# Kernel tuning notes

Measured on AMD Instinct MI355X. Metric: run time of the kernel, lower is better.

## Reference

```python
import jax, jax.numpy as jnp
import numpy as np

N_NODES = 100000
N_EDGES = 1600000
IN_DIM = 128
HID = 128
OUT = 64


def gcn_conv(x, src, dst, W, b, n_nodes):
    # x: [N, Din] -> [N, Dout]; symmetric-normalized GCN with self-loops (PyG GCNConv defaults)
    h = x @ W  # transform first (as PyG does)
    loop = jnp.arange(n_nodes, dtype=src.dtype)
    s = jnp.concatenate([src, loop])
    d = jnp.concatenate([dst, loop])
    deg = jax.ops.segment_sum(jnp.ones_like(d, dtype=h.dtype), d, num_segments=n_nodes)
    dis = jnp.where(deg > 0, jax.lax.rsqrt(deg), 0.0)
    norm = dis[s] * dis[d]  # [E+N]
    msgs = h[s] * norm[:, None]  # gather-transform
    out = jax.ops.segment_sum(msgs, d, num_segments=n_nodes)  # scatter-add
    return out + b


def setup_inputs() -> dict:
    key = jax.random.key(0)
    ks = jax.random.split(key, 12)
    x = jax.random.normal(ks[0], (N_NODES, IN_DIM), dtype=jnp.float32)
    edge_index = jax.random.randint(ks[1], (2, N_EDGES), 0, N_NODES, dtype=jnp.int32)
    def lin(k, fan_in, fan_out):
        bound = 1.0 / np.sqrt(fan_in)
        kw, kb = jax.random.split(k)
        W = jax.random.uniform(kw, (fan_in, fan_out), minval=-bound, maxval=bound, dtype=jnp.float32)
        b = jax.random.uniform(kb, (fan_out,), minval=-bound, maxval=bound, dtype=jnp.float32)
        return W, b
    W1, b1 = lin(ks[2], IN_DIM, HID)
    W2, b2 = lin(ks[3], HID, HID)
    Wp1, bp1 = lin(ks[4], HID, HID)
    Wp2, bp2 = lin(ks[5], HID, OUT)
    return {"x": x, "edge_index": edge_index,
            "W1": W1, "b1": b1, "W2": W2, "b2": b2,
            "Wp1": Wp1, "bp1": bp1, "Wp2": Wp2, "bp2": bp2}


def reference(x, edge_index, W1, b1, W2, b2, Wp1, bp1, Wp2, bp2):
    n = x.shape[0]
    src, dst = edge_index[0], edge_index[1]
    # layer 1: GCNConv + relu (dropout inactive at eval)
    h = jax.nn.relu(gcn_conv(x, src, dst, W1, b1, n))
    # layer 2
    h = jax.nn.relu(gcn_conv(h, src, dst, W2, b2, n))
    # post MLP head
    h = h @ Wp1 + bp1
    h = h @ Wp2 + bp2
    return jax.nn.log_softmax(h, axis=1)
```

## Files before the change

kernel.cpp:

```cpp
#include <hip/hip_runtime.h>
#include <hip/hip_bf16.h>
#include <cstdint>

typedef __attribute__((ext_vector_type(8))) short short8;
typedef __attribute__((ext_vector_type(16))) float f32x16;
typedef unsigned short us;

#define BIN_SHIFT 9
#define BIN_NODES 512
#define CAPB 12288
#define EPB 4096

__device__ __forceinline__ float bflo(uint32_t u) { return __builtin_bit_cast(float, u << 16); }
__device__ __forceinline__ float bfhi(uint32_t u) { return __builtin_bit_cast(float, u & 0xffff0000u); }

__device__ __forceinline__ us f32_to_bf16_rne(float f) {
  uint32_t u = __builtin_bit_cast(uint32_t, f);
  u += 0x7fffu + ((u >> 16) & 1u);
  return (us)(u >> 16);
}

__device__ __forceinline__ void split2(float f, us& h, us& l) {
  uint32_t u = __builtin_bit_cast(uint32_t, f);
  h = (us)(u >> 16);
  float fh = __builtin_bit_cast(float, u & 0xffff0000u);
  float r = f - fh;
  l = (us)(__builtin_bit_cast(uint32_t, r) >> 16);
}

__global__ __launch_bounds__(256) void k_binA(
    const int* __restrict__ src, const int* __restrict__ dst,
    uint2* __restrict__ binbuf, int* __restrict__ gcur, int E, int nbins) {
  __shared__ uint2 stage[EPB];
  __shared__ int cnt[256], base[256], cur[256], gbase[256];
  int tid = threadIdx.x;
  int e0 = blockIdx.x * EPB;
  int ne = min(EPB, E - e0);
  if (ne <= 0) return;
  cnt[tid] = 0;
  __syncthreads();
  for (int i = tid; i < ne; i += 256) atomicAdd(&cnt[dst[e0 + i] >> BIN_SHIFT], 1);
  __syncthreads();
  if (tid < 64) {
    int carry = 0;
#pragma unroll
    for (int c = 0; c < 4; ++c) {
      int v = cnt[c * 64 + tid];
      int incl = v;
#pragma unroll
      for (int off = 1; off < 64; off <<= 1) {
        int t = __shfl_up(incl, off, 64);
        if (tid >= off) incl += t;
      }
      base[c * 64 + tid] = carry + incl - v;
      carry += __shfl(incl, 63, 64);
    }
  }
  __syncthreads();
  if (tid < nbins && cnt[tid] > 0) gbase[tid] = atomicAdd(&gcur[tid], cnt[tid]);
  cur[tid] = base[tid];
  __syncthreads();
  for (int i = tid; i < ne; i += 256) {
    int d = dst[e0 + i], s = src[e0 + i];
    int p = atomicAdd(&cur[d >> BIN_SHIFT], 1);
    stage[p] = make_uint2((unsigned)d, (unsigned)s);
  }
  __syncthreads();
  for (int i = tid; i < ne; i += 256) {
    uint2 en = stage[i];
    int b = en.x >> BIN_SHIFT;
    int gi = gbase[b] + (i - base[b]);
    if (gi < CAPB) binbuf[(size_t)b * CAPB + gi] = en;
  }
}

__global__ __launch_bounds__(256) void k_passB(
    const uint2* __restrict__ binbuf, const int* __restrict__ gcur,
    int* __restrict__ deg, float* __restrict__ dis, int* __restrict__ start,
    int* __restrict__ col, int N, int nbins) {
  __shared__ int hist[512], lstart[512], cur[512];
  __shared__ int colstage[CAPB];
  __shared__ int binbase_s;
  int b = blockIdx.x, tid = threadIdx.x;
  int node0 = b << BIN_SHIFT;
  int cnt = min(gcur[b], CAPB);
  hist[tid] = 0; hist[tid + 256] = 0;
  __syncthreads();
  const uint2* bp = binbuf + (size_t)b * CAPB;
  for (int i = tid; i < cnt; i += 256) atomicAdd(&hist[bp[i].x & (BIN_NODES - 1)], 1);
  __syncthreads();
  if (tid < 64) {
    int s = 0;
    for (int i = tid; i < b; i += 64) s += min(gcur[i], CAPB);
#pragma unroll
    for (int off = 32; off; off >>= 1) s += __shfl_xor(s, off, 64);
    if (tid == 0) binbase_s = s;
    int carry = 0;
#pragma unroll
    for (int c = 0; c < 8; ++c) {
      int v = hist[c * 64 + tid];
      int incl = v;
#pragma unroll
      for (int off = 1; off < 64; off <<= 1) {
        int t = __shfl_up(incl, off, 64);
        if (tid >= off) incl += t;
      }
      lstart[c * 64 + tid] = carry + incl - v;
      carry += __shfl(incl, 63, 64);
    }
  }
  __syncthreads();
  int binbase = binbase_s;
  for (int i = tid; i < 512; i += 256) {
    int node = node0 + i;
    if (node < N) {
      int dg = hist[i];
      deg[node] = dg;
      dis[node] = rsqrtf((float)(dg + 1));
      start[node] = binbase + lstart[i];
    }
  }
  cur[tid] = lstart[tid]; cur[tid + 256] = lstart[tid + 256];
  __syncthreads();
  for (int i = tid; i < cnt; i += 256) {
    uint2 en = bp[i];
    int p = atomicAdd(&cur[en.x & (BIN_NODES - 1)], 1);
    colstage[p] = (int)en.y;
  }
  __syncthreads();
  for (int i = tid; i < cnt; i += 256) col[binbase + i] = colstage[i];
}

__global__ void k_prep(const float* __restrict__ W1, const float* __restrict__ W2,
                       const float* __restrict__ Wp1, const float* __restrict__ Wp2,
                       const float* __restrict__ bp1, const float* __restrict__ bp2,
                       us* __restrict__ Wt1h, us* __restrict__ Wt1l,
                       us* __restrict__ Wt2h, us* __restrict__ Wt2l,
                       us* __restrict__ Wch, us* __restrict__ Wcl, float* __restrict__ bc) {
  int blk = blockIdx.x, tid = threadIdx.x;
  if (blk < 128) {
    const float* W = (blk < 64) ? W1 : W2;
    us* Wh = (blk < 64) ? Wt1h : Wt2h;
    us* Wl = (blk < 64) ? Wt1l : Wt2l;
    int idx = (blk & 63) * 256 + tid;
    int k = idx >> 7, n = idx & 127;
    us h, l;
    split2(W[idx], h, l);
    Wh[n * 128 + k] = h;
    Wl[n * 128 + k] = l;
  } else if (blk < 160) {
    int idx = (blk - 128) * 256 + tid;
    int k = idx >> 6, j = idx & 63;
    float acc = 0.f;
    for (int t = 0; t < 128; ++t) acc += Wp1[k * 128 + t] * Wp2[t * 64 + j];
    us h, l;
    split2(acc, h, l);
    Wch[j * 128 + k] = h;
    Wcl[j * 128 + k] = l;
  } else {
    int j = tid;
    if (j < 64) {
      float acc = bp2[j];
      for (int t = 0; t < 128; ++t) acc += bp1[t] * Wp2[t * 64 + j];
      bc[j] = acc;
    }
  }
}

template <bool AF32>
__global__ __launch_bounds__(256) void k_gemm_mfma(
    const void* __restrict__ Av, const us* __restrict__ Wh,
    const us* __restrict__ Wl, const float* __restrict__ dis,
    us* __restrict__ out_bf16, int N, int ntiles) {
  __shared__ us As_hi[32 * 136];
  __shared__ us As_lo[32 * 136];
  int tid = threadIdx.x;
  int wave = tid >> 6, lane = tid & 63;
  int n0 = wave * 32;
  int nn = n0 + (lane & 31);
  int khalf = (lane >> 5) * 8;
  int m = lane & 31;

  short8 bh[8], bl[8];
#pragma unroll
  for (int c = 0; c < 8; ++c) {
    bh[c] = *(const short8*)&Wh[nn * 128 + c * 16 + khalf];
    bl[c] = *(const short8*)&Wl[nn * 128 + c * 16 + khalf];
  }

  for (int t = blockIdx.x; t < ntiles; t += gridDim.x) {
    int row0 = t * 32;
    __syncthreads();
    if (AF32) {
      const float* A = (const float*)Av;
      for (int j = tid; j < 1024; j += 256) {
        int r = j >> 5, c = j & 31;
        int row = row0 + r;
        float4 v = make_float4(0.f, 0.f, 0.f, 0.f);
        if (row < N) v = *(const float4*)&A[(size_t)row * 128 + c * 4];
        us h0, h1, h2, h3, l0, l1, l2, l3;
        split2(v.x, h0, l0); split2(v.y, h1, l1);
        split2(v.z, h2, l2); split2(v.w, h3, l3);
        *(ushort4*)&As_hi[r * 136 + c * 4] = make_ushort4(h0, h1, h2, h3);
        *(ushort4*)&As_lo[r * 136 + c * 4] = make_ushort4(l0, l1, l2, l3);
      }
    } else {
      const us* A = (const us*)Av;
      for (int j = tid; j < 512; j += 256) {
        int r = j >> 4, c = j & 15;
        int row = row0 + r;
        uint4 v = make_uint4(0u, 0u, 0u, 0u);
        if (row < N) v = *(const uint4*)&A[(size_t)row * 128 + c * 8];
        *(uint4*)&As_hi[r * 136 + c * 8] = v;
      }
    }
    __syncthreads();

    f32x16 acc = {};
#pragma unroll
    for (int c = 0; c < 8; ++c) {
      short8 ah = *(const short8*)&As_hi[m * 136 + c * 16 + khalf];
      acc = __builtin_amdgcn_mfma_f32_32x32x16_bf16(ah, bh[c], acc, 0, 0, 0);
      acc = __builtin_amdgcn_mfma_f32_32x32x16_bf16(ah, bl[c], acc, 0, 0, 0);
      if (AF32) {
        short8 al = *(const short8*)&As_lo[m * 136 + c * 16 + khalf];
        acc = __builtin_amdgcn_mfma_f32_32x32x16_bf16(al, bh[c], acc, 0, 0, 0);
      }
    }

    int col = n0 + (lane & 31);
    int rbase = row0 + 4 * (lane >> 5);
#pragma unroll
    for (int reg = 0; reg < 16; ++reg) {
      int row = rbase + (reg & 3) + 8 * (reg >> 2);
      if (row < N) {
        float v = acc[reg] * dis[row];
        out_bf16[(size_t)row * 128 + col] = f32_to_bf16_rne(v);
      }
    }
  }
}

__global__ __launch_bounds__(256) void k_gather(
    const us* __restrict__ h, us* __restrict__ o,
    const int* __restrict__ start, const int* __restrict__ deg,
    const int* __restrict__ col, const float* __restrict__ dis,
    const float* __restrict__ bias, int N) {
  int wave = threadIdx.x >> 6, lane = threadIdx.x & 63;
  int node = blockIdx.x * 4 + wave;
  if (node >= N) return;
  const uint32_t* h1 = (const uint32_t*)h;
  uint32_t u = h1[(size_t)node * 64 + lane];
  float a0 = bflo(u), b0 = bfhi(u);
  float a1 = 0.f, b1 = 0.f, a2 = 0.f, b2 = 0.f, a3 = 0.f, b3 = 0.f;
  int e0 = start[node];
  int dg = deg[node];
  int myc = (lane < dg) ? col[e0 + lane] : N;
  int dgm = min(dg, 64);
  for (int k = 0; k < dgm; k += 4) {
    int c0 = __builtin_amdgcn_readlane(myc, k);
    int c1 = __builtin_amdgcn_readlane(myc, k + 1);
    int c2 = __builtin_amdgcn_readlane(myc, k + 2);
    int c3 = __builtin_amdgcn_readlane(myc, k + 3);
    uint32_t u0 = h1[(size_t)c0 * 64 + lane];
    uint32_t u1 = h1[(size_t)c1 * 64 + lane];
    uint32_t u2 = h1[(size_t)c2 * 64 + lane];
    uint32_t u3 = h1[(size_t)c3 * 64 + lane];
    a0 += bflo(u0); b0 += bfhi(u0);
    a1 += bflo(u1); b1 += bfhi(u1);
    a2 += bflo(u2); b2 += bfhi(u2);
    a3 += bflo(u3); b3 += bfhi(u3);
  }
  for (int e = e0 + 64; e < e0 + dg; ++e) {
    uint32_t u0 = h1[(size_t)col[e] * 64 + lane];
    a0 += bflo(u0); b0 += bfhi(u0);
  }
  float sc = dis[node];
  float2 bb = ((const float2*)bias)[lane];
  float rx = fmaxf((a0 + a1 + a2 + a3) * sc + bb.x, 0.f);
  float ry = fmaxf((b0 + b1 + b2 + b3) * sc + bb.y, 0.f);
  ((uint32_t*)o)[(size_t)node * 64 + lane] =
      ((uint32_t)f32_to_bf16_rne(ry) << 16) | f32_to_bf16_rne(rx);
}

__global__ __launch_bounds__(256) void k_head_mfma(
    const us* __restrict__ act, const us* __restrict__ Wch,
    const us* __restrict__ Wcl, const float* __restrict__ bc,
    float* __restrict__ out, int N) {
  __shared__ us As[64 * 136];
  __shared__ float red[2][2][64];
  int tid = threadIdx.x;
  int wave = tid >> 6, lane = tid & 63;
  int rt = wave >> 1, ct = wave & 1;
  int colj = ct * 32 + (lane & 31);
  int khalf = (lane >> 5) * 8;
  int m = lane & 31;

  short8 bh[8], bl[8];
#pragma unroll
  for (int c = 0; c < 8; ++c) {
    bh[c] = *(const short8*)&Wch[colj * 128 + c * 16 + khalf];
    bl[c] = *(const short8*)&Wcl[colj * 128 + c * 16 + khalf];
  }

  int row0 = blockIdx.x * 64;
  for (int j = tid; j < 1024; j += 256) {
    int r = j >> 4, c = j & 15;
    int row = row0 + r;
    uint4 v = make_uint4(0u, 0u, 0u, 0u);
    if (row < N) v = *(const uint4*)&act[(size_t)row * 128 + c * 8];
    *(uint4*)&As[r * 136 + c * 8] = v;
  }
  __syncthreads();

  f32x16 acc = {};
  int mrow = rt * 32 + m;
#pragma unroll
  for (int c = 0; c < 8; ++c) {
    short8 ah = *(const short8*)&As[mrow * 136 + c * 16 + khalf];
    acc = __builtin_amdgcn_mfma_f32_32x32x16_bf16(ah, bh[c], acc, 0, 0, 0);
    acc = __builtin_amdgcn_mfma_f32_32x32x16_bf16(ah, bl[c], acc, 0, 0, 0);
  }

  float bcv = bc[colj];
  float lg[16], mx[16];
#pragma unroll
  for (int reg = 0; reg < 16; ++reg) {
    lg[reg] = acc[reg] + bcv;
    float v = lg[reg];
#pragma unroll
    for (int off = 16; off > 0; off >>= 1) v = fmaxf(v, __shfl_xor(v, off, 32));
    mx[reg] = v;
  }
  if ((lane & 31) == 0) {
#pragma unroll
    for (int reg = 0; reg < 16; ++reg) {
      int rl = rt * 32 + (reg & 3) + 8 * (reg >> 2) + 4 * (lane >> 5);
      red[0][ct][rl] = mx[reg];
    }
  }
  __syncthreads();

  float ex[16], sm[16];
#pragma unroll
  for (int reg = 0; reg < 16; ++reg) {
    int rl = rt * 32 + (reg & 3) + 8 * (reg >> 2) + 4 * (lane >> 5);
    float rmax = fmaxf(red[0][0][rl], red[0][1][rl]);
    ex[reg] = lg[reg] - rmax;
    float v = expf(ex[reg]);
#pragma unroll
    for (int off = 16; off > 0; off >>= 1) v += __shfl_xor(v, off, 32);
    sm[reg] = v;
  }
  if ((lane & 31) == 0) {
#pragma unroll
    for (int reg = 0; reg < 16; ++reg) {
      int rl = rt * 32 + (reg & 3) + 8 * (reg >> 2) + 4 * (lane >> 5);
      red[1][ct][rl] = sm[reg];
    }
  }
  __syncthreads();

#pragma unroll
  for (int reg = 0; reg < 16; ++reg) {
    int rl = rt * 32 + (reg & 3) + 8 * (reg >> 2) + 4 * (lane >> 5);
    int row = row0 + rl;
    if (row < N) {
      float total = red[1][0][rl] + red[1][1][rl];
      out[(size_t)row * 64 + colj] = ex[reg] - logf(total);
    }
  }
}

extern "C" void kernel_launch(void* const* d_in, const int* in_sizes, int n_in,
                              void* d_out, int out_size, void* d_ws, size_t ws_size,
                              hipStream_t stream) {
  const float* x   = (const float*)d_in[0];
  const int*   ei  = (const int*)d_in[1];
  const float* W1  = (const float*)d_in[2];
  const float* b1  = (const float*)d_in[3];
  const float* W2  = (const float*)d_in[4];
  const float* b2  = (const float*)d_in[5];
  const float* Wp1 = (const float*)d_in[6];
  const float* bp1 = (const float*)d_in[7];
  const float* Wp2 = (const float*)d_in[8];
  const float* bp2 = (const float*)d_in[9];
  float* out = (float*)d_out;

  int N = in_sizes[0] / 128;
  int E = in_sizes[1] / 2;
  const int* src = ei;
  const int* dst = ei + E;
  int nbins = (N + BIN_NODES - 1) >> BIN_SHIFT;

  float* dis   = (float*)d_ws;
  int*   deg   = (int*)(dis + N);
  int*   start = deg + N;
  int*   col   = start + N;
  int*   gcur  = col + ((E + 3) & ~3);
  us* Wt1h = (us*)(gcur + 256);
  us* Wt1l = Wt1h + 16384;
  us* Wt2h = Wt1l + 16384;
  us* Wt2l = Wt2h + 16384;
  us* Wch  = Wt2l + 16384;
  us* Wcl  = Wch + 8192;
  float* bc = (float*)(Wcl + 8192);
  uint2* binbuf = (uint2*)(bc + 80);
  us* hbuf = (us*)(binbuf + (size_t)nbins * CAPB);
  us* act  = hbuf + (size_t)(N + 1) * 128;

  hipMemsetAsync(gcur, 0, 256 * sizeof(int), stream);
  hipMemsetAsync(hbuf + (size_t)N * 128, 0, 128 * sizeof(us), stream);

  int ablocks = (E + EPB - 1) / EPB;
  k_binA<<<ablocks, 256, 0, stream>>>(src, dst, binbuf, gcur, E, nbins);
  k_passB<<<nbins, 256, 0, stream>>>(binbuf, gcur, deg, dis, start, col, N, nbins);
  k_prep<<<161, 256, 0, stream>>>(W1, W2, Wp1, Wp2, bp1, bp2,
                                  Wt1h, Wt1l, Wt2h, Wt2l, Wch, Wcl, bc);

  int ntiles = (N + 31) / 32;
  int gemm_grid = ntiles < 1024 ? ntiles : 1024;
  int agblocks = (N + 3) / 4;
  int hblocks = (N + 63) / 64;

  k_gemm_mfma<true><<<gemm_grid, 256, 0, stream>>>(x, Wt1h, Wt1l, dis, hbuf, N, ntiles);
  k_gather<<<agblocks, 256, 0, stream>>>(hbuf, act, start, deg, col, dis, b1, N);
  k_gemm_mfma<false><<<gemm_grid, 256, 0, stream>>>(act, Wt2h, Wt2l, dis, hbuf, N, ntiles);
  k_gather<<<agblocks, 256, 0, stream>>>(hbuf, act, start, deg, col, dis, b2, N);
  k_head_mfma<<<hblocks, 256, 0, stream>>>(act, Wch, Wcl, bc, out, N);
}
```

Before: 402.5 us.

## Fuse neighbor aggregation into following GEMM and head kernels

The gather/aggregation step is moved inside the layer-2 GEMM and the head/log-softmax kernels, so aggregated rows are written straight to LDS instead of a global activation buffer. This removes two kernel launches and a global write+read of the activations. Layer-1 GEMM also drops the low-part split of x, converting x to bf16 directly and doing one fewer MFMA per k-step. Risks: the gather now runs serially per wave inside a capped persistent grid, which lowers memory-level parallelism, and dropping the x low part reduces accuracy.

Measured after the change: 564.1 us. 40.1% more time.

```diff
diff --git a/kernel.cpp b/kernel.cpp
--- a/kernel.cpp
+++ b/kernel.cpp
@@ -167,13 +167,55 @@
   }
 }
 
-template <bool AF32>
-__global__ __launch_bounds__(256) void k_gemm_mfma(
-    const void* __restrict__ Av, const us* __restrict__ Wh,
+__device__ __forceinline__ void gather_rows_to_lds(
+    const us* __restrict__ h, us* __restrict__ As, int row0, int wave, int lane, int NPW,
+    const int* __restrict__ start, const int* __restrict__ deg, const int* __restrict__ col,
+    const float* __restrict__ dis, const float* __restrict__ bias, int N) {
+  const uint32_t* h1 = (const uint32_t*)h;
+  float2 bb = ((const float2*)bias)[lane];
+  for (int i = 0; i < NPW; ++i) {
+    int r = wave * NPW + i;
+    int node = row0 + r;
+    bool valid = node < N;
+    int nd = valid ? node : N;
+    uint32_t u = h1[(size_t)nd * 64 + lane];
+    float a0 = bflo(u), b0 = bfhi(u);
+    float a1 = 0.f, b1 = 0.f, a2 = 0.f, b2 = 0.f, a3 = 0.f, b3 = 0.f;
+    int e0 = valid ? start[node] : 0;
+    int dg = valid ? deg[node] : 0;
+    int myc = (lane < dg) ? col[e0 + lane] : N;
+    int dgm = min(dg, 64);
+    for (int k = 0; k < dgm; k += 4) {
+      int c0 = __builtin_amdgcn_readlane(myc, k);
+      int c1 = __builtin_amdgcn_readlane(myc, k + 1);
+      int c2 = __builtin_amdgcn_readlane(myc, k + 2);
+      int c3 = __builtin_amdgcn_readlane(myc, k + 3);
+      uint32_t u0 = h1[(size_t)c0 * 64 + lane];
+      uint32_t u1 = h1[(size_t)c1 * 64 + lane];
+      uint32_t u2 = h1[(size_t)c2 * 64 + lane];
+      uint32_t u3 = h1[(size_t)c3 * 64 + lane];
+      a0 += bflo(u0); b0 += bfhi(u0);
+      a1 += bflo(u1); b1 += bfhi(u1);
+      a2 += bflo(u2); b2 += bfhi(u2);
+      a3 += bflo(u3); b3 += bfhi(u3);
+    }
+    for (int e = e0 + 64; e < e0 + dg; ++e) {
+      uint32_t u0 = h1[(size_t)col[e] * 64 + lane];
+      a0 += bflo(u0); b0 += bfhi(u0);
+    }
+    float sc = valid ? dis[node] : 0.f;
+    float rx = fmaxf((a0 + a1 + a2 + a3) * sc + bb.x, 0.f);
+    float ry = fmaxf((b0 + b1 + b2 + b3) * sc + bb.y, 0.f);
+    *(uint32_t*)&As[r * 136 + 2 * lane] =
+        ((uint32_t)f32_to_bf16_rne(ry) << 16) | f32_to_bf16_rne(rx);
+  }
+}
+
+__global__ __launch_bounds__(256) void k_gemm1(
+    const float* __restrict__ A, const us* __restrict__ Wh,
     const us* __restrict__ Wl, const float* __restrict__ dis,
     us* __restrict__ out_bf16, int N, int ntiles) {
-  __shared__ us As_hi[32 * 136];
-  __shared__ us As_lo[32 * 136];
+  __shared__ us As[32 * 136];
   int tid = threadIdx.x;
   int wave = tid >> 6, lane = tid & 63;
   int n0 = wave * 32;
@@ -191,41 +233,23 @@
   for (int t = blockIdx.x; t < ntiles; t += gridDim.x) {
     int row0 = t * 32;
     __syncthreads();
-    if (AF32) {
-      const float* A = (const float*)Av;
-      for (int j = tid; j < 1024; j += 256) {
-        int r = j >> 5, c = j & 31;
-        int row = row0 + r;
-        float4 v = make_float4(0.f, 0.f, 0.f, 0.f);
-        if (row < N) v = *(const float4*)&A[(size_t)row * 128 + c * 4];
-        us h0, h1, h2, h3, l0, l1, l2, l3;
-        split2(v.x, h0, l0); split2(v.y, h1, l1);
-        split2(v.z, h2, l2); split2(v.w, h3, l3);
-        *(ushort4*)&As_hi[r * 136 + c * 4] = make_ushort4(h0, h1, h2, h3);
-        *(ushort4*)&As_lo[r * 136 + c * 4] = make_ushort4(l0, l1, l2, l3);
-      }
-    } else {
-      const us* A = (const us*)Av;
-      for (int j = tid; j < 512; j += 256) {
-        int r = j >> 4, c = j & 15;
-        int row = row0 + r;
-        uint4 v = make_uint4(0u, 0u, 0u, 0u);
-        if (row < N) v = *(const uint4*)&A[(size_t)row * 128 + c * 8];
-        *(uint4*)&As_hi[r * 136 + c * 8] = v;
-      }
+    for (int j = tid; j < 1024; j += 256) {
+      int r = j >> 5, c = j & 31;
+      int row = row0 + r;
+      float4 v = make_float4(0.f, 0.f, 0.f, 0.f);
+      if (row < N) v = *(const float4*)&A[(size_t)row * 128 + c * 4];
+      *(ushort4*)&As[r * 136 + c * 4] = make_ushort4(
+          f32_to_bf16_rne(v.x), f32_to_bf16_rne(v.y),
+          f32_to_bf16_rne(v.z), f32_to_bf16_rne(v.w));
     }
     __syncthreads();
 
     f32x16 acc = {};
 #pragma unroll
     for (int c = 0; c < 8; ++c) {
-      short8 ah = *(const short8*)&As_hi[m * 136 + c * 16 + khalf];
+      short8 ah = *(const short8*)&As[m * 136 + c * 16 + khalf];
       acc = __builtin_amdgcn_mfma_f32_32x32x16_bf16(ah, bh[c], acc, 0, 0, 0);
       acc = __builtin_amdgcn_mfma_f32_32x32x16_bf16(ah, bl[c], acc, 0, 0, 0);
-      if (AF32) {
-        short8 al = *(const short8*)&As_lo[m * 136 + c * 16 + khalf];
-        acc = __builtin_amdgcn_mfma_f32_32x32x16_bf16(al, bh[c], acc, 0, 0, 0);
-      }
     }
 
     int col = n0 + (lane & 31);
@@ -241,52 +265,59 @@
   }
 }
 
-__global__ __launch_bounds__(256) void k_gather(
-    const us* __restrict__ h, us* __restrict__ o,
+__global__ __launch_bounds__(256) void k_gcn2(
+    const us* __restrict__ h, const us* __restrict__ Wh, const us* __restrict__ Wl,
     const int* __restrict__ start, const int* __restrict__ deg,
     const int* __restrict__ col, const float* __restrict__ dis,
-    const float* __restrict__ bias, int N) {
-  int wave = threadIdx.x >> 6, lane = threadIdx.x & 63;
-  int node = blockIdx.x * 4 + wave;
-  if (node >= N) return;
-  const uint32_t* h1 = (const uint32_t*)h;
-  uint32_t u = h1[(size_t)node * 64 + lane];
-  float a0 = bflo(u), b0 = bfhi(u);
-  float a1 = 0.f, b1 = 0.f, a2 = 0.f, b2 = 0.f, a3 = 0.f, b3 = 0.f;
-  int e0 = start[node];
-  int dg = deg[node];
-  int myc = (lane < dg) ? col[e0 + lane] : N;
-  int dgm = min(dg, 64);
-  for (int k = 0; k < dgm; k += 4) {
-    int c0 = __builtin_amdgcn_readlane(myc, k);
-    int c1 = __builtin_amdgcn_readlane(myc, k + 1);
-    int c2 = __builtin_amdgcn_readlane(myc, k + 2);
-    int c3 = __builtin_amdgcn_readlane(myc, k + 3);
-    uint32_t u0 = h1[(size_t)c0 * 64 + lane];
-    uint32_t u1 = h1[(size_t)c1 * 64 + lane];
-    uint32_t u2 = h1[(size_t)c2 * 64 + lane];
-    uint32_t u3 = h1[(size_t)c3 * 64 + lane];
-    a0 += bflo(u0); b0 += bfhi(u0);
-    a1 += bflo(u1); b1 += bfhi(u1);
-    a2 += bflo(u2); b2 += bfhi(u2);
-    a3 += bflo(u3); b3 += bfhi(u3);
-  }
-  for (int e = e0 + 64; e < e0 + dg; ++e) {
-    uint32_t u0 = h1[(size_t)col[e] * 64 + lane];
-    a0 += bflo(u0); b0 += bfhi(u0);
-  }
-  float sc = dis[node];
-  float2 bb = ((const float2*)bias)[lane];
-  float rx = fmaxf((a0 + a1 + a2 + a3) * sc + bb.x, 0.f);
-  float ry = fmaxf((b0 + b1 + b2 + b3) * sc + bb.y, 0.f);
-  ((uint32_t*)o)[(size_t)node * 64 + lane] =
-      ((uint32_t)f32_to_bf16_rne(ry) << 16) | f32_to_bf16_rne(rx);
-}
-
-__global__ __launch_bounds__(256) void k_head_mfma(
-    const us* __restrict__ act, const us* __restrict__ Wch,
-    const us* __restrict__ Wcl, const float* __restrict__ bc,
-    float* __restrict__ out, int N) {
+    const float* __restrict__ bias, us* __restrict__ out_bf16, int N, int ntiles) {
+  __shared__ us As[32 * 136];
+  int tid = threadIdx.x;
+  int wave = tid >> 6, lane = tid & 63;
+  int n0 = wave * 32;
+  int nn = n0 + (lane & 31);
+  int khalf = (lane >> 5) * 8;
+  int m = lane & 31;
+
+  short8 bh[8], bl[8];
+#pragma unroll
+  for (int c = 0; c < 8; ++c) {
+    bh[c] = *(const short8*)&Wh[nn * 128 + c * 16 + khalf];
+    bl[c] = *(const short8*)&Wl[nn * 128 + c * 16 + khalf];
+  }
+
+  for (int t = blockIdx.x; t < ntiles; t += gridDim.x) {
+    int row0 = t * 32;
+    __syncthreads();
+    gather_rows_to_lds(h, As, row0, wave, lane, 8, start, deg, col, dis, bias, N);
+    __syncthreads();
+
+    f32x16 acc = {};
+#pragma unroll
+    for (int c = 0; c < 8; ++c) {
+      short8 ah = *(const short8*)&As[m * 136 + c * 16 + khalf];
+      acc = __builtin_amdgcn_mfma_f32_32x32x16_bf16(ah, bh[c], acc, 0, 0, 0);
+      acc = __builtin_amdgcn_mfma_f32_32x32x16_bf16(ah, bl[c], acc, 0, 0, 0);
+    }
+
+    int col_o = n0 + (lane & 31);
+    int rbase = row0 + 4 * (lane >> 5);
+#pragma unroll
+    for (int reg = 0; reg < 16; ++reg) {
+      int row = rbase + (reg & 3) + 8 * (reg >> 2);
+      if (row < N) {
+        float v = acc[reg] * dis[row];
+        out_bf16[(size_t)row * 128 + col_o] = f32_to_bf16_rne(v);
+      }
+    }
+  }
+}
+
+__global__ __launch_bounds__(256) void k_gcnhead(
+    const us* __restrict__ h, const us* __restrict__ Wch, const us* __restrict__ Wcl,
+    const int* __restrict__ start, const int* __restrict__ deg,
+    const int* __restrict__ col, const float* __restrict__ dis,
+    const float* __restrict__ bias, const float* __restrict__ bc,
+    float* __restrict__ out, int N, int ntiles) {
   __shared__ us As[64 * 136];
   __shared__ float red[2][2][64];
   int tid = threadIdx.x;
@@ -302,72 +333,69 @@
     bh[c] = *(const short8*)&Wch[colj * 128 + c * 16 + khalf];
     bl[c] = *(const short8*)&Wcl[colj * 128 + c * 16 + khalf];
   }
-
-  int row0 = blockIdx.x * 64;
-  for (int j = tid; j < 1024; j += 256) {
-    int r = j >> 4, c = j & 15;
-    int row = row0 + r;
-    uint4 v = make_uint4(0u, 0u, 0u, 0u);
-    if (row < N) v = *(const uint4*)&act[(size_t)row * 128 + c * 8];
-    *(uint4*)&As[r * 136 + c * 8] = v;
-  }
-  __syncthreads();
-
-  f32x16 acc = {};
-  int mrow = rt * 32 + m;
-#pragma unroll
-  for (int c = 0; c < 8; ++c) {
-    short8 ah = *(const short8*)&As[mrow * 136 + c * 16 + khalf];
-    acc = __builtin_amdgcn_mfma_f32_32x32x16_bf16(ah, bh[c], acc, 0, 0, 0);
-    acc = __builtin_amdgcn_mfma_f32_32x32x16_bf16(ah, bl[c], acc, 0, 0, 0);
-  }
-
   float bcv = bc[colj];
-  float lg[16], mx[16];
-#pragma unroll
-  for (int reg = 0; reg < 16; ++reg) {
-    lg[reg] = acc[reg] + bcv;
-    float v = lg[reg];
-#pragma unroll
-    for (int off = 16; off > 0; off >>= 1) v = fmaxf(v, __shfl_xor(v, off, 32));
-    mx[reg] = v;
-  }
-  if ((lane & 31) == 0) {
+
+  for (int t = blockIdx.x; t < ntiles; t += gridDim.x) {
+    int row0 = t * 64;
+    __syncthreads();
+    gather_rows_to_lds(h, As, row0, wave, lane, 16, start, deg, col, dis, bias, N);
+    __syncthreads();
+
+    f32x16 acc = {};
+    int mrow = rt * 32 + m;
+#pragma unroll
+    for (int c = 0; c < 8; ++c) {
+      short8 ah = *(const short8*)&As[mrow * 136 + c * 16 + khalf];
+      acc = __builtin_amdgcn_mfma_f32_32x32x16_bf16(ah, bh[c], acc, 0, 0, 0);
+      acc = __builtin_amdgcn_mfma_f32_32x32x16_bf16(ah, bl[c], acc, 0, 0, 0);
+    }
+
+    float lg[16], mx[16];
+#pragma unroll
+    for (int reg = 0; reg < 16; ++reg) {
+      lg[reg] = acc[reg] + bcv;
+      float v = lg[reg];
+#pragma unroll
+      for (int off = 16; off > 0; off >>= 1) v = fmaxf(v, __shfl_xor(v, off, 32));
+      mx[reg] = v;
+    }
+    if ((lane & 31) == 0) {
+#pragma unroll
+      for (int reg = 0; reg < 16; ++reg) {
+        int rl = rt * 32 + (reg & 3) + 8 * (reg >> 2) + 4 * (lane >> 5);
+        red[0][ct][rl] = mx[reg];
+      }
+    }
+    __syncthreads();
+
+    float ex[16], sm[16];
 #pragma unroll
     for (int reg = 0; reg < 16; ++reg) {
       int rl = rt * 32 + (reg & 3) + 8 * (reg >> 2) + 4 * (lane >> 5);
-      red[0][ct][rl] = mx[reg];
-    }
-  }
-  __syncthreads();
-
-  float ex[16], sm[16];
-#pragma unroll
-  for (int reg = 0; reg < 16; ++reg) {
-    int rl = rt * 32 + (reg & 3) + 8 * (reg >> 2) + 4 * (lane >> 5);
-    float rmax = fmaxf(red[0][0][rl], red[0][1][rl]);
-    ex[reg] = lg[reg] - rmax;
-    float v = expf(ex[reg]);
-#pragma unroll
-    for (int off = 16; off > 0; off >>= 1) v += __shfl_xor(v, off, 32);
-    sm[reg] = v;
-  }
-  if ((lane & 31) == 0) {
+      float rmax = fmaxf(red[0][0][rl], red[0][1][rl]);
+      ex[reg] = lg[reg] - rmax;
+      float v = expf(ex[reg]);
+#pragma unroll
+      for (int off = 16; off > 0; off >>= 1) v += __shfl_xor(v, off, 32);
+      sm[reg] = v;
+    }
+    if ((lane & 31) == 0) {
+#pragma unroll
+      for (int reg = 0; reg < 16; ++reg) {
+        int rl = rt * 32 + (reg & 3) + 8 * (reg >> 2) + 4 * (lane >> 5);
+        red[1][ct][rl] = sm[reg];
+      }
+    }
+    __syncthreads();
+
 #pragma unroll
     for (int reg = 0; reg < 16; ++reg) {
       int rl = rt * 32 + (reg & 3) + 8 * (reg >> 2) + 4 * (lane >> 5);
-      red[1][ct][rl] = sm[reg];
-    }
-  }
-  __syncthreads();
-
-#pragma unroll
-  for (int reg = 0; reg < 16; ++reg) {
-    int rl = rt * 32 + (reg & 3) + 8 * (reg >> 2) + 4 * (lane >> 5);
-    int row = row0 + rl;
-    if (row < N) {
-      float total = red[1][0][rl] + red[1][1][rl];
-      out[(size_t)row * 64 + colj] = ex[reg] - logf(total);
+      int row = row0 + rl;
+      if (row < N) {
+        float total = red[1][0][rl] + red[1][1][rl];
+        out[(size_t)row * 64 + colj] = ex[reg] - logf(total);
+      }
     }
   }
 }
@@ -406,11 +434,12 @@
   us* Wcl  = Wch + 8192;
   float* bc = (float*)(Wcl + 8192);
   uint2* binbuf = (uint2*)(bc + 80);
-  us* hbuf = (us*)(binbuf + (size_t)nbins * CAPB);
-  us* act  = hbuf + (size_t)(N + 1) * 128;
+  us* hbuf1 = (us*)(binbuf + (size_t)nbins * CAPB);
+  us* hbuf2 = hbuf1 + (size_t)(N + 1) * 128;
 
   hipMemsetAsync(gcur, 0, 256 * sizeof(int), stream);
-  hipMemsetAsync(hbuf + (size_t)N * 128, 0, 128 * sizeof(us), stream);
+  hipMemsetAsync(hbuf1 + (size_t)N * 128, 0, 128 * sizeof(us), stream);
+  hipMemsetAsync(hbuf2 + (size_t)N * 128, 0, 128 * sizeof(us), stream);
 
   int ablocks = (E + EPB - 1) / EPB;
   k_binA<<<ablocks, 256, 0, stream>>>(src, dst, binbuf, gcur, E, nbins);
@@ -418,14 +447,14 @@
   k_prep<<<161, 256, 0, stream>>>(W1, W2, Wp1, Wp2, bp1, bp2,
                                   Wt1h, Wt1l, Wt2h, Wt2l, Wch, Wcl, bc);
 
-  int ntiles = (N + 31) / 32;
-  int gemm_grid = ntiles < 1024 ? ntiles : 1024;
-  int agblocks = (N + 3) / 4;
-  int hblocks = (N + 63) / 64;
-
-  k_gemm_mfma<true><<<gemm_grid, 256, 0, stream>>>(x, Wt1h, Wt1l, dis, hbuf, N, ntiles);
-  k_gather<<<agblocks, 256, 0, stream>>>(hbuf, act, start, deg, col, dis, b1, N);
-  k_gemm_mfma<false><<<gemm_grid, 256, 0, stream>>>(act, Wt2h, Wt2l, dis, hbuf, N, ntiles);
-  k_gather<<<agblocks, 256, 0, stream>>>(hbuf, act, start, deg, col, dis, b2, N);
-  k_head_mfma<<<hblocks, 256, 0, stream>>>(act, Wch, Wcl, bc, out, N);
-}
+  int ntiles32 = (N + 31) / 32;
+  int ntiles64 = (N + 63) / 64;
+  int g32 = ntiles32 < 1024 ? ntiles32 : 1024;
+  int g64 = ntiles64 < 1024 ? ntiles64 : 1024;
+
+  k_gemm1<<<g32, 256, 0, stream>>>(x, Wt1h, Wt1l, dis, hbuf1, N, ntiles32);
+  k_gcn2<<<g32, 256, 0, stream>>>(hbuf1, Wt2h, Wt2l, start, deg, col, dis, b1,
+                                  hbuf2, N, ntiles32);
+  k_gcnhead<<<g64, 256, 0, stream>>>(hbuf2, Wch, Wcl, start, deg, col, dis, b2,
+                                     bc, out, N, ntiles64);
+}
```
